# Kernel optimization log

Measured on AMD Instinct MI355X. Metric: run time of the kernel, lower is better.

The kernel has to match this reference:

```python
import jax, jax.numpy as jnp
import numpy as np

BETA = 0.25


def setup_inputs() -> dict:
    key = jax.random.key(0)
    k1, k2 = jax.random.split(key)
    inputs = jax.random.normal(k1, (32, 4096, 64), dtype=jnp.float32)
    # VarianceScaling(uniform) ~ small-magnitude init; plain normal scaled works for a numeric reference
    codebook = jax.random.normal(k2, (1024, 64), dtype=jnp.float32) * (1.0 / np.sqrt(64.0))
    return {"inputs": inputs, "codebook": codebook}


def reference(inputs, codebook):
    D = codebook.shape[-1]
    flat = jnp.reshape(inputs, (-1, D))                      # [N, D]
    flat_sqr = jnp.sum(flat ** 2, axis=-1, keepdims=True)    # [N, 1]
    code_sqr = jnp.sum(codebook ** 2, axis=-1)[None, :]      # [1, K]
    # full pairwise squared distances [N, K]
    distances = flat_sqr - 2.0 * (flat @ codebook.T) + code_sqr
    encoding_indices = jnp.reshape(jnp.argmin(distances, axis=-1), inputs.shape[:-1])
    quantize = codebook[encoding_indices]                    # gather -> [..., D]
    encoding_loss = jnp.mean((jax.lax.stop_gradient(inputs) - quantize) ** 2)
    commit_loss = jnp.mean((inputs - jax.lax.stop_gradient(quantize)) ** 2)
    loss = encoding_loss + BETA * commit_loss
    # straight-through estimator
    z_q = inputs + jax.lax.stop_gradient(quantize - inputs)
    return loss, z_q, encoding_indices
```

## Files before the change

### kernel.cpp

```cpp
#include <hip/hip_runtime.h>

#define N_ROWS 131072
#define D 64
#define K_CODES 1024

typedef _Float16 f16x8 __attribute__((ext_vector_type(8)));
typedef _Float16 f16x4 __attribute__((ext_vector_type(4)));
typedef float    f32x4 __attribute__((ext_vector_type(4)));

__global__ void csqr_kernel(const float* __restrict__ CB,
                            float* __restrict__ csqr,
                            float* __restrict__ loss) {
    int k = blockIdx.x * 256 + threadIdx.x;
    if (k == 0) *loss = 0.0f;
    if (k >= K_CODES) return;
    const float4* p = (const float4*)(CB + (size_t)k * D);
    float s = 0.0f;
#pragma unroll
    for (int i = 0; i < D / 4; ++i) {
        float4 v = p[i];
        s += v.x * v.x + v.y * v.y + v.z * v.z + v.w * v.w;
    }
    csqr[k] = s;
}

__global__ __launch_bounds__(256, 2)
void argmin_kernel(const float* __restrict__ X, const float* __restrict__ CB,
                   const float* __restrict__ csqr,
                   int* __restrict__ idx_out, float* __restrict__ idxf_out) {
    __shared__ __align__(16) _Float16 Bs[64][136];

    const int t    = threadIdx.x;
    const int wave = t >> 6;
    const int lane = t & 63;
    const int lrow = lane & 15;
    const int quad = lane >> 4;

    const int R0 = blockIdx.x * 256 + wave * 64;

    f16x8 Ah[4][2], Al[4][2];
#pragma unroll
    for (int mt = 0; mt < 4; ++mt) {
        const float* xr = X + (size_t)(R0 + mt * 16 + lrow) * D;
#pragma unroll
        for (int ks = 0; ks < 2; ++ks) {
            const int k0 = ks * 32 + quad * 8;
            float4 v0 = *(const float4*)(xr + k0);
            float4 v1 = *(const float4*)(xr + k0 + 4);
            float xs[8] = {v0.x, v0.y, v0.z, v0.w, v1.x, v1.y, v1.z, v1.w};
            f16x8 h, l;
#pragma unroll
            for (int j = 0; j < 8; ++j) {
                _Float16 hj = (_Float16)xs[j];
                h[j] = hj;
                l[j] = (_Float16)(xs[j] - (float)hj);
            }
            Ah[mt][ks] = h;
            Al[mt][ks] = l;
        }
    }

    float bestd[4][4];
    int   besti[4][4];
#pragma unroll
    for (int mt = 0; mt < 4; ++mt)
#pragma unroll
        for (int r = 0; r < 4; ++r) { bestd[mt][r] = 3.0e38f; besti[mt][r] = 0; }

    for (int chunk = 0; chunk < K_CODES / 64; ++chunk) {
        __syncthreads();
#pragma unroll
        for (int i = 0; i < 4; ++i) {
            int q    = i * 256 + t;
            int code = q >> 4;
            int kq   = (q & 15) * 4;
            float4 v = *(const float4*)(CB + (size_t)(chunk * 64 + code) * D + kq);
            f16x4 h, l;
            h[0] = (_Float16)v.x; l[0] = (_Float16)(v.x - (float)h[0]);
            h[1] = (_Float16)v.y; l[1] = (_Float16)(v.y - (float)h[1]);
            h[2] = (_Float16)v.z; l[2] = (_Float16)(v.z - (float)h[2]);
            h[3] = (_Float16)v.w; l[3] = (_Float16)(v.w - (float)h[3]);
            *(f16x4*)&Bs[code][kq]      = h;
            *(f16x4*)&Bs[code][64 + kq] = l;
        }
        __syncthreads();

#pragma unroll
        for (int ct = 0; ct < 4; ++ct) {
            const _Float16* bp = &Bs[ct * 16 + lrow][quad * 8];
            f16x8 Bh0 = *(const f16x8*)(bp);
            f16x8 Bh1 = *(const f16x8*)(bp + 32);
            f16x8 Bl0 = *(const f16x8*)(bp + 64);
            f16x8 Bl1 = *(const f16x8*)(bp + 96);
            const int   c  = chunk * 64 + ct * 16 + lrow;
            const float cs = csqr[c];
#pragma unroll
            for (int mt = 0; mt < 4; ++mt) {
                f32x4 acc = {0.f, 0.f, 0.f, 0.f};
                acc = __builtin_amdgcn_mfma_f32_16x16x32_f16(Ah[mt][0], Bh0, acc, 0, 0, 0);
                acc = __builtin_amdgcn_mfma_f32_16x16x32_f16(Ah[mt][1], Bh1, acc, 0, 0, 0);
                acc = __builtin_amdgcn_mfma_f32_16x16x32_f16(Al[mt][0], Bh0, acc, 0, 0, 0);
                acc = __builtin_amdgcn_mfma_f32_16x16x32_f16(Al[mt][1], Bh1, acc, 0, 0, 0);
                acc = __builtin_amdgcn_mfma_f32_16x16x32_f16(Ah[mt][0], Bl0, acc, 0, 0, 0);
                acc = __builtin_amdgcn_mfma_f32_16x16x32_f16(Ah[mt][1], Bl1, acc, 0, 0, 0);
                acc = __builtin_amdgcn_mfma_f32_16x16x32_f16(Al[mt][0], Bl0, acc, 0, 0, 0);
                acc = __builtin_amdgcn_mfma_f32_16x16x32_f16(Al[mt][1], Bl1, acc, 0, 0, 0);
#pragma unroll
                for (int r = 0; r < 4; ++r) {
                    float s = fmaf(-2.0f, acc[r], cs);
                    if (s < bestd[mt][r]) { bestd[mt][r] = s; besti[mt][r] = c; }
                }
            }
        }
    }

#pragma unroll
    for (int mt = 0; mt < 4; ++mt)
#pragma unroll
        for (int r = 0; r < 4; ++r) {
            float d = bestd[mt][r];
            int   i = besti[mt][r];
#pragma unroll
            for (int m = 1; m < 16; m <<= 1) {
                float od = __shfl_xor(d, m, 64);
                int   oi = __shfl_xor(i, m, 64);
                if (od < d || (od == d && oi < i)) { d = od; i = oi; }
            }
            if (lrow == 0) {
                int row = R0 + mt * 16 + quad * 4 + r;
                idx_out[row]  = i;
                idxf_out[row] = (float)i;
            }
        }
}

__global__ __launch_bounds__(256)
void gather_kernel(const float* __restrict__ X, const float* __restrict__ CB,
                   const int* __restrict__ idx,
                   float* __restrict__ zq, float* __restrict__ loss) {
    const int tid    = blockIdx.x * 256 + threadIdx.x;
    const int nquads = N_ROWS * (D / 4);
    const int stride = gridDim.x * 256;
    float acc = 0.0f;
    for (int q = tid; q < nquads; q += stride) {
        int row = q >> 4;
        int d4  = q & 15;
        int k   = idx[row];
        float4 x = ((const float4*)X)[q];
        float4 c = ((const float4*)(CB + (size_t)k * D))[d4];
        ((float4*)zq)[q] = c;
        float dx = x.x - c.x, dy = x.y - c.y, dz = x.z - c.z, dw = x.w - c.w;
        acc += dx * dx + dy * dy + dz * dz + dw * dw;
    }
    __shared__ float red[256];
    red[threadIdx.x] = acc;
    __syncthreads();
    for (int s = 128; s > 0; s >>= 1) {
        if (threadIdx.x < s) red[threadIdx.x] += red[threadIdx.x + s];
        __syncthreads();
    }
    if (threadIdx.x == 0)
        atomicAdd(loss, red[0] * (1.25f / (float)(N_ROWS * D)));
}

extern "C" void kernel_launch(void* const* d_in, const int* in_sizes, int n_in,
                              void* d_out, int out_size, void* d_ws,
                              size_t ws_size, hipStream_t stream) {
    const float* X  = (const float*)d_in[0];
    const float* CB = (const float*)d_in[1];

    float* out  = (float*)d_out;
    float* loss = out;
    float* zq   = out + 1;
    float* idxf = out + 1 + (size_t)N_ROWS * D;

    float* csqr = (float*)d_ws;
    int*   idx  = (int*)((char*)d_ws + 4096);

    hipLaunchKernelGGL(csqr_kernel, dim3(4), dim3(256), 0, stream,
                       CB, csqr, loss);
    hipLaunchKernelGGL(argmin_kernel, dim3(N_ROWS / 256), dim3(256), 0, stream,
                       X, CB, csqr, idx, idxf);
    hipLaunchKernelGGL(gather_kernel, dim3(2048), dim3(256), 0, stream,
                       X, CB, idx, zq, loss);
}
```

Measured before the change: 175.4 us.

## Fuse gather and loss into argmin, precompute split-f16 codebook, prefetch chunks

Precomputes the hi/lo f16 split of the codebook once in a prep kernel and fuses the gather, z_q write and loss computation into the argmin kernel, removing the third launch and the re-read of X. The argmin loop register-prefetches the next codebook chunk, seeds the accumulator with the code norm, folds the -2 factor into the input split, drops the lo*lo MFMA terms and halves rows per block so occupancy can rise. The loss is computed algebraically as sum of x^2 plus the minimum distance, which adds rounding risk against the direct difference sum.

```diff
diff --git a/kernel.cpp b/kernel.cpp
--- a/kernel.cpp
+++ b/kernel.cpp
@@ -3,44 +3,59 @@
 #define N_ROWS 131072
 #define D 64
 #define K_CODES 1024
+#define MT 2
+#define ROWS_PER_BLOCK 128
+#define NCHUNK (K_CODES / 64)
 
 typedef _Float16 f16x8 __attribute__((ext_vector_type(8)));
-typedef _Float16 f16x4 __attribute__((ext_vector_type(4)));
 typedef float    f32x4 __attribute__((ext_vector_type(4)));
 
-__global__ void csqr_kernel(const float* __restrict__ CB,
-                            float* __restrict__ csqr,
-                            float* __restrict__ loss) {
+__global__ __launch_bounds__(256)
+void prep_kernel(const float* __restrict__ CB, _Float16* __restrict__ CBs,
+                 float* __restrict__ csqr, float* __restrict__ loss) {
     int k = blockIdx.x * 256 + threadIdx.x;
     if (k == 0) *loss = 0.0f;
     if (k >= K_CODES) return;
     const float4* p = (const float4*)(CB + (size_t)k * D);
+    _Float16* hi = CBs + (size_t)k * 128;
+    _Float16* lo = hi + 64;
     float s = 0.0f;
 #pragma unroll
-    for (int i = 0; i < D / 4; ++i) {
+    for (int i = 0; i < 16; ++i) {
         float4 v = p[i];
         s += v.x * v.x + v.y * v.y + v.z * v.z + v.w * v.w;
+        float vv[4] = {v.x, v.y, v.z, v.w};
+#pragma unroll
+        for (int j = 0; j < 4; ++j) {
+            _Float16 h = (_Float16)vv[j];
+            hi[i * 4 + j] = h;
+            lo[i * 4 + j] = (_Float16)(vv[j] - (float)h);
+        }
     }
     csqr[k] = s;
 }
 
-__global__ __launch_bounds__(256, 2)
-void argmin_kernel(const float* __restrict__ X, const float* __restrict__ CB,
+__global__ __launch_bounds__(256, 4)
+void argmin_kernel(const float* __restrict__ X,
+                   const _Float16* __restrict__ CBs,
                    const float* __restrict__ csqr,
-                   int* __restrict__ idx_out, float* __restrict__ idxf_out) {
+                   const float* __restrict__ CB,
+                   float* __restrict__ zq, float* __restrict__ idxf,
+                   float* __restrict__ loss) {
     __shared__ __align__(16) _Float16 Bs[64][136];
+    __shared__ float LsC[K_CODES];
 
     const int t    = threadIdx.x;
     const int wave = t >> 6;
     const int lane = t & 63;
     const int lrow = lane & 15;
     const int quad = lane >> 4;
+    const int R0   = blockIdx.x * ROWS_PER_BLOCK + wave * (MT * 16);
 
-    const int R0 = blockIdx.x * 256 + wave * 64;
-
-    f16x8 Ah[4][2], Al[4][2];
+    f16x8 Ah[MT][2], Al[MT][2];
+    float xsq = 0.0f;
 #pragma unroll
-    for (int mt = 0; mt < 4; ++mt) {
+    for (int mt = 0; mt < MT; ++mt) {
         const float* xr = X + (size_t)(R0 + mt * 16 + lrow) * D;
 #pragma unroll
         for (int ks = 0; ks < 2; ++ks) {
@@ -51,39 +66,43 @@
             f16x8 h, l;
 #pragma unroll
             for (int j = 0; j < 8; ++j) {
-                _Float16 hj = (_Float16)xs[j];
-                h[j] = hj;
-                l[j] = (_Float16)(xs[j] - (float)hj);
+                xsq += xs[j] * xs[j];
+                float sv = -2.0f * xs[j];
+                _Float16 hh = (_Float16)sv;
+                h[j] = hh;
+                l[j] = (_Float16)(sv - (float)hh);
             }
             Ah[mt][ks] = h;
             Al[mt][ks] = l;
         }
     }
 
-    float bestd[4][4];
-    int   besti[4][4];
+    ((float4*)LsC)[t] = ((const float4*)csqr)[t];
+
+    float bestd[MT][4];
+    int   besti[MT][4];
 #pragma unroll
-    for (int mt = 0; mt < 4; ++mt)
+    for (int mt = 0; mt < MT; ++mt)
 #pragma unroll
         for (int r = 0; r < 4; ++r) { bestd[mt][r] = 3.0e38f; besti[mt][r] = 0; }
 
-    for (int chunk = 0; chunk < K_CODES / 64; ++chunk) {
-        __syncthreads();
+    const f16x8* gB = (const f16x8*)CBs;
+    f16x8 pf[4];
+#pragma unroll
+    for (int i = 0; i < 4; ++i) pf[i] = gB[i * 256 + t];
+
+    for (int chunk = 0; chunk < NCHUNK; ++chunk) {
 #pragma unroll
         for (int i = 0; i < 4; ++i) {
-            int q    = i * 256 + t;
-            int code = q >> 4;
-            int kq   = (q & 15) * 4;
-            float4 v = *(const float4*)(CB + (size_t)(chunk * 64 + code) * D + kq);
-            f16x4 h, l;
-            h[0] = (_Float16)v.x; l[0] = (_Float16)(v.x - (float)h[0]);
-            h[1] = (_Float16)v.y; l[1] = (_Float16)(v.y - (float)h[1]);
-            h[2] = (_Float16)v.z; l[2] = (_Float16)(v.z - (float)h[2]);
-            h[3] = (_Float16)v.w; l[3] = (_Float16)(v.w - (float)h[3]);
-            *(f16x4*)&Bs[code][kq]      = h;
-            *(f16x4*)&Bs[code][64 + kq] = l;
+            int q = i * 256 + t, code = q >> 4, u = q & 15;
+            *(f16x8*)&Bs[code][u * 8] = pf[i];
         }
         __syncthreads();
+        if (chunk + 1 < NCHUNK) {
+#pragma unroll
+            for (int i = 0; i < 4; ++i)
+                pf[i] = gB[(chunk + 1) * 1024 + i * 256 + t];
+        }
 
 #pragma unroll
         for (int ct = 0; ct < 4; ++ct) {
@@ -93,74 +112,58 @@
             f16x8 Bl0 = *(const f16x8*)(bp + 64);
             f16x8 Bl1 = *(const f16x8*)(bp + 96);
             const int   c  = chunk * 64 + ct * 16 + lrow;
-            const float cs = csqr[c];
+            const float cs = LsC[c];
 #pragma unroll
-            for (int mt = 0; mt < 4; ++mt) {
-                f32x4 acc = {0.f, 0.f, 0.f, 0.f};
+            for (int mt = 0; mt < MT; ++mt) {
+                f32x4 acc = {cs, cs, cs, cs};
                 acc = __builtin_amdgcn_mfma_f32_16x16x32_f16(Ah[mt][0], Bh0, acc, 0, 0, 0);
                 acc = __builtin_amdgcn_mfma_f32_16x16x32_f16(Ah[mt][1], Bh1, acc, 0, 0, 0);
                 acc = __builtin_amdgcn_mfma_f32_16x16x32_f16(Al[mt][0], Bh0, acc, 0, 0, 0);
                 acc = __builtin_amdgcn_mfma_f32_16x16x32_f16(Al[mt][1], Bh1, acc, 0, 0, 0);
                 acc = __builtin_amdgcn_mfma_f32_16x16x32_f16(Ah[mt][0], Bl0, acc, 0, 0, 0);
                 acc = __builtin_amdgcn_mfma_f32_16x16x32_f16(Ah[mt][1], Bl1, acc, 0, 0, 0);
-                acc = __builtin_amdgcn_mfma_f32_16x16x32_f16(Al[mt][0], Bl0, acc, 0, 0, 0);
-                acc = __builtin_amdgcn_mfma_f32_16x16x32_f16(Al[mt][1], Bl1, acc, 0, 0, 0);
 #pragma unroll
                 for (int r = 0; r < 4; ++r) {
-                    float s = fmaf(-2.0f, acc[r], cs);
-                    if (s < bestd[mt][r]) { bestd[mt][r] = s; besti[mt][r] = c; }
+                    bool lt = acc[r] < bestd[mt][r];
+                    bestd[mt][r] = lt ? acc[r] : bestd[mt][r];
+                    besti[mt][r] = lt ? c : besti[mt][r];
                 }
             }
         }
+        __syncthreads();
     }
 
+    const float scale = 1.25f / (float)((size_t)N_ROWS * D);
+
 #pragma unroll
-    for (int mt = 0; mt < 4; ++mt)
+    for (int m = 1; m < 64; m <<= 1) xsq += __shfl_xor(xsq, m, 64);
+    if (lane == 0) atomicAdd(loss, xsq * scale);
+
+    float ssum = 0.0f;
+#pragma unroll
+    for (int mt = 0; mt < MT; ++mt) {
 #pragma unroll
         for (int r = 0; r < 4; ++r) {
-            float d = bestd[mt][r];
-            int   i = besti[mt][r];
+            float dv = bestd[mt][r];
+            int   iv = besti[mt][r];
 #pragma unroll
             for (int m = 1; m < 16; m <<= 1) {
-                float od = __shfl_xor(d, m, 64);
-                int   oi = __shfl_xor(i, m, 64);
-                if (od < d || (od == d && oi < i)) { d = od; i = oi; }
+                float od = __shfl_xor(dv, m, 64);
+                int   oi = __shfl_xor(iv, m, 64);
+                if (od < dv || (od == dv && oi < iv)) { dv = od; iv = oi; }
             }
+            int row = R0 + mt * 16 + quad * 4 + r;
             if (lrow == 0) {
-                int row = R0 + mt * 16 + quad * 4 + r;
-                idx_out[row]  = i;
-                idxf_out[row] = (float)i;
+                idxf[row] = (float)iv;
+                ssum += dv;
             }
+            float4 cv = *(const float4*)(CB + (size_t)iv * D + lrow * 4);
+            *(float4*)(zq + (size_t)row * D + lrow * 4) = cv;
         }
-}
-
-__global__ __launch_bounds__(256)
-void gather_kernel(const float* __restrict__ X, const float* __restrict__ CB,
-                   const int* __restrict__ idx,
-                   float* __restrict__ zq, float* __restrict__ loss) {
-    const int tid    = blockIdx.x * 256 + threadIdx.x;
-    const int nquads = N_ROWS * (D / 4);
-    const int stride = gridDim.x * 256;
-    float acc = 0.0f;
-    for (int q = tid; q < nquads; q += stride) {
-        int row = q >> 4;
-        int d4  = q & 15;
-        int k   = idx[row];
-        float4 x = ((const float4*)X)[q];
-        float4 c = ((const float4*)(CB + (size_t)k * D))[d4];
-        ((float4*)zq)[q] = c;
-        float dx = x.x - c.x, dy = x.y - c.y, dz = x.z - c.z, dw = x.w - c.w;
-        acc += dx * dx + dy * dy + dz * dz + dw * dw;
     }
-    __shared__ float red[256];
-    red[threadIdx.x] = acc;
-    __syncthreads();
-    for (int s = 128; s > 0; s >>= 1) {
-        if (threadIdx.x < s) red[threadIdx.x] += red[threadIdx.x + s];
-        __syncthreads();
-    }
-    if (threadIdx.x == 0)
-        atomicAdd(loss, red[0] * (1.25f / (float)(N_ROWS * D)));
+    ssum += __shfl_xor(ssum, 16, 64);
+    ssum += __shfl_xor(ssum, 32, 64);
+    if (lane == 0) atomicAdd(loss, ssum * scale);
 }
 
 extern "C" void kernel_launch(void* const* d_in, const int* in_sizes, int n_in,
@@ -174,13 +177,11 @@
     float* zq   = out + 1;
     float* idxf = out + 1 + (size_t)N_ROWS * D;
 
-    float* csqr = (float*)d_ws;
-    int*   idx  = (int*)((char*)d_ws + 4096);
+    float*    csqr = (float*)d_ws;
+    _Float16* CBs  = (_Float16*)((char*)d_ws + 4096);
 
-    hipLaunchKernelGGL(csqr_kernel, dim3(4), dim3(256), 0, stream,
-                       CB, csqr, loss);
-    hipLaunchKernelGGL(argmin_kernel, dim3(N_ROWS / 256), dim3(256), 0, stream,
-                       X, CB, csqr, idx, idxf);
-    hipLaunchKernelGGL(gather_kernel, dim3(2048), dim3(256), 0, stream,
-                       X, CB, idx, zq, loss);
+    hipLaunchKernelGGL(prep_kernel, dim3(4), dim3(256), 0, stream,
+                       CB, CBs, csqr, loss);
+    hipLaunchKernelGGL(argmin_kernel, dim3(N_ROWS / ROWS_PER_BLOCK), dim3(256),
+                       0, stream, X, CBs, csqr, CB, zq, idxf, loss);
 }
```

Result: slower. 217.2 us (+23.8%).
